# Performance work log

Hardware: AMD Instinct MI355X
Metric: run time of the kernel (lower is better)

## Reference

```python
import jax, jax.numpy as jnp
import numpy as np
import math

D_MODEL = 1024
NHEAD = 16
SEQ_LEN = 4096
K_PROJ = 16
HEAD_DIM = D_MODEL // NHEAD


def setup_inputs() -> dict:
    key = jax.random.key(0)
    ks = jax.random.split(key, 11)
    x = jax.random.normal(ks[0], (4, SEQ_LEN, D_MODEL), dtype=jnp.float32)
    s = 1.0 / math.sqrt(D_MODEL)
    Wq = jax.random.uniform(ks[1], (D_MODEL, D_MODEL), minval=-s, maxval=s)
    bq = jax.random.uniform(ks[2], (D_MODEL,), minval=-s, maxval=s)
    Wk = jax.random.uniform(ks[3], (D_MODEL, D_MODEL), minval=-s, maxval=s)
    bk = jax.random.uniform(ks[4], (D_MODEL,), minval=-s, maxval=s)
    Wv = jax.random.uniform(ks[5], (D_MODEL, D_MODEL), minval=-s, maxval=s)
    bv = jax.random.uniform(ks[6], (D_MODEL,), minval=-s, maxval=s)
    Wo = jax.random.uniform(ks[7], (D_MODEL, D_MODEL), minval=-s, maxval=s)
    bo = jax.random.uniform(ks[8], (D_MODEL,), minval=-s, maxval=s)
    E = jax.random.normal(ks[9], (NHEAD, K_PROJ, SEQ_LEN)) * 0.02
    F = jax.random.normal(ks[10], (NHEAD, K_PROJ, SEQ_LEN)) * 0.02
    return {"x": x, "Wq": Wq, "bq": bq, "Wk": Wk, "bk": bk,
            "Wv": Wv, "bv": bv, "Wo": Wo, "bo": bo, "E": E, "F": F}


def reference(x, Wq, bq, Wk, bk, Wv, bv, Wo, bo, E, F):
    B, N, D = x.shape
    # torch Linear: y = x @ W.T + b
    q = x @ Wq.T + bq
    k = x @ Wk.T + bk
    v = x @ Wv.T + bv
    # [B, H, N, Dh]
    def split_heads(t):
        return t.reshape(B, N, NHEAD, HEAD_DIM).transpose(0, 2, 1, 3)
    q, k, v = split_heads(q), split_heads(k), split_heads(v)
    # low-rank projections of K, V along sequence: [B, H, Kp, Dh]
    k_lin = jnp.einsum('bhnd,hkn->bhkd', k, E)
    v_lin = jnp.einsum('bhnd,hkn->bhkd', v, F)
    scores = jnp.einsum('bhnd,bhkd->bhnk', q, k_lin) / math.sqrt(HEAD_DIM)
    attn = jax.nn.softmax(scores, axis=-1)  # dropout is identity in eval
    out = jnp.einsum('bhnk,bhkd->bhnd', attn, v_lin)
    out = out.transpose(0, 2, 1, 3).reshape(B, N, D)
    return out @ Wo.T + bo
```

## Files before the change

### kernel.cpp

```cpp
#include <hip/hip_runtime.h>
#include <hip/hip_bf16.h>

#define SEQLEN 4096

typedef __bf16 bf16x8 __attribute__((ext_vector_type(8)));
typedef float f32x4 __attribute__((ext_vector_type(4)));
typedef __attribute__((ext_vector_type(8))) unsigned short u16x8;

__device__ inline float bf2f(unsigned short s) {
  union { unsigned u; float f; } t; t.u = ((unsigned)s) << 16; return t.f;
}
__device__ inline unsigned short f2bf(float f) {
  __hip_bfloat16 h = __float2bfloat16(f);
  return *reinterpret_cast<unsigned short*>(&h);
}

__device__ inline void gload_lds16(const void* g, void* l) {
  __builtin_amdgcn_global_load_lds(
      (const __attribute__((address_space(1))) unsigned int*)g,
      (__attribute__((address_space(3))) unsigned int*)l, 16, 0, 0);
}

__global__ void cvt_all(const float* __restrict__ x, const float* __restrict__ Wq,
                        const float* __restrict__ Wk, const float* __restrict__ Wv,
                        const float* __restrict__ Wo,
                        const float* __restrict__ bq, const float* __restrict__ bk,
                        const float* __restrict__ bv,
                        unsigned short* __restrict__ Xb,
                        unsigned short* __restrict__ Wqkv,
                        unsigned short* __restrict__ WoB, float* __restrict__ Bqkv) {
  long i = (long)blockIdx.x * 256 + threadIdx.x;
  const float* src;
  unsigned short* dst;
  long rel;
  if (i < 4194304) {
    src = x; dst = Xb; rel = i;
  } else if (i < 4456448) {
    src = Wq; dst = Wqkv; rel = i - 4194304;
  } else if (i < 4718592) {
    src = Wk; dst = Wqkv + 1048576; rel = i - 4456448;
  } else if (i < 4980736) {
    src = Wv; dst = Wqkv + 2097152; rel = i - 4718592;
  } else if (i < 5242880) {
    src = Wo; dst = WoB; rel = i - 4980736;
  } else if (i < 5243648) {
    long j = i - 5242880;
    const float* bsrc = (j < 256) ? bq : (j < 512) ? bk : bv;
    long jr = j & 255;
    reinterpret_cast<float4*>(Bqkv)[j] =
        reinterpret_cast<const float4*>(bsrc)[jr];
    return;
  } else {
    return;
  }
  float4 v = reinterpret_cast<const float4*>(src)[rel];
  ushort4 o;
  o.x = f2bf(v.x); o.y = f2bf(v.y); o.z = f2bf(v.z); o.w = f2bf(v.w);
  reinterpret_cast<ushort4*>(dst)[rel] = o;
}


#define MFMA16(mk, A00, A01, A10, A11)                                          \
  __builtin_amdgcn_s_setprio(1);                                                \
  _Pragma("unroll")                                                             \
  for (int n = 0; n < 4; ++n)                                                   \
    acc[2*(mk)][n]   = __builtin_amdgcn_mfma_f32_16x16x32_bf16(A00, b[n][0], acc[2*(mk)][n],   0, 0, 0); \
  _Pragma("unroll")                                                             \
  for (int n = 0; n < 4; ++n)                                                   \
    acc[2*(mk)+1][n] = __builtin_amdgcn_mfma_f32_16x16x32_bf16(A10, b[n][0], acc[2*(mk)+1][n], 0, 0, 0); \
  _Pragma("unroll")                                                             \
  for (int n = 0; n < 4; ++n)                                                   \
    acc[2*(mk)][n]   = __builtin_amdgcn_mfma_f32_16x16x32_bf16(A01, b[n][1], acc[2*(mk)][n],   0, 0, 0); \
  _Pragma("unroll")                                                             \
  for (int n = 0; n < 4; ++n)                                                   \
    acc[2*(mk)+1][n] = __builtin_amdgcn_mfma_f32_16x16x32_bf16(A11, b[n][1], acc[2*(mk)+1][n], 0, 0, 0); \
  __builtin_amdgcn_s_setprio(0);

#define LDA8(mi, sg) (*reinterpret_cast<const bf16x8*>(&as[((wr << 7) + (mi) * 16 + r16) * 64 + (sg) * 8]))
#define LDB8(ni, sg) (*reinterpret_cast<const bf16x8*>(&bs[((wc << 6) + (ni) * 16 + r16) * 64 + (sg) * 8]))

template <typename OUT_T>
__global__ __launch_bounds__(512, 2) void gemm8p(
    const unsigned short* __restrict__ A, const unsigned short* __restrict__ B,
    const float* __restrict__ bias, OUT_T* __restrict__ C, int M, int N, int K,
    int ldc) {
  extern __shared__ __align__(16) unsigned short lds[];

  const int tid = threadIdx.x;
  const int lane = tid & 63, wv = tid >> 6;
  const int wr = wv >> 2, wc = wv & 3;
  const int r16 = lane & 15, kg = lane >> 4;
  const int sg0 = (0 * 4 + kg) ^ (r16 & 7);
  const int sg1 = (1 * 4 + kg) ^ (r16 & 7);

  const int xcd = (int)blockIdx.x & 7;
  const int pos = (int)blockIdx.x >> 3;
  const int rpx = (M >> 8) >> 3;
  const int tile_m = xcd * rpx + (pos % rpx);
  const int tile_n = pos / rpx;
  const int brow = tile_m << 8, bcol = tile_n << 8;

  const unsigned short* Ag = A + (size_t)brow * K;
  const unsigned short* Bg = B + (size_t)bcol * K;

  const int sr = tid >> 3;
  const int sc = tid & 7;
  const int sgl = sc ^ (sr & 7);

  auto STG = [&](const unsigned short* G, unsigned short* dstbuf, int row0, int kt) {
    gload_lds16(G + (size_t)(row0 + sr) * K + (size_t)kt * 64 + sgl * 8,
                dstbuf + (row0 + sr) * 64 + sc * 8);
  };

  f32x4 acc[8][4];
#pragma unroll
  for (int m = 0; m < 8; ++m)
#pragma unroll
    for (int n = 0; n < 4; ++n) acc[m][n] = (f32x4)0.0f;

  {
    unsigned short* a0 = lds;
    unsigned short* b0 = lds + 32768;
    STG(Bg, b0, 0, 0);   STG(Bg, b0, 64, 0);
    STG(Bg, b0, 128, 0); STG(Bg, b0, 192, 0);
    STG(Ag, a0, 0, 0);   STG(Ag, a0, 128, 0);
    STG(Ag, a0, 64, 0);  STG(Ag, a0, 192, 0);
  }
  asm volatile("s_waitcnt vmcnt(2)" ::: "memory");
  __builtin_amdgcn_s_barrier();

  const int NT = K >> 6;
  for (int t = 0; t < NT; ++t) {
    const int cur = t & 1;
    const unsigned short* as = lds + (cur << 14);
    const unsigned short* bs = lds + 32768 + (cur << 14);
    unsigned short* an = lds + ((cur ^ 1) << 14);
    unsigned short* bn = lds + 32768 + ((cur ^ 1) << 14);
    const int tn = (t + 1 < NT) ? t + 1 : 0;

    bf16x8 b[4][2];
#pragma unroll
    for (int n = 0; n < 4; ++n) { b[n][0] = LDB8(n, sg0); b[n][1] = LDB8(n, sg1); }

    {
      bf16x8 a00 = LDA8(0, sg0), a01 = LDA8(0, sg1);
      bf16x8 a10 = LDA8(1, sg0), a11 = LDA8(1, sg1);
      STG(Bg, bn, 0, tn);   STG(Bg, bn, 64, tn);
      STG(Bg, bn, 128, tn); STG(Bg, bn, 192, tn);
      __builtin_amdgcn_s_barrier();
      MFMA16(0, a00, a01, a10, a11);
      __builtin_amdgcn_s_barrier();
    }
    {
      bf16x8 a00 = LDA8(2, sg0), a01 = LDA8(2, sg1);
      bf16x8 a10 = LDA8(3, sg0), a11 = LDA8(3, sg1);
      STG(Ag, an, 0, tn); STG(Ag, an, 128, tn);
      __builtin_amdgcn_s_barrier();
      MFMA16(1, a00, a01, a10, a11);
      asm volatile("s_waitcnt vmcnt(6)" ::: "memory");
      __builtin_amdgcn_s_barrier();
    }
    {
      bf16x8 a00 = LDA8(4, sg0), a01 = LDA8(4, sg1);
      bf16x8 a10 = LDA8(5, sg0), a11 = LDA8(5, sg1);
      STG(Ag, an, 64, tn); STG(Ag, an, 192, tn);
      __builtin_amdgcn_s_barrier();
      MFMA16(2, a00, a01, a10, a11);
      __builtin_amdgcn_s_barrier();
    }
    {
      bf16x8 a00 = LDA8(6, sg0), a01 = LDA8(6, sg1);
      bf16x8 a10 = LDA8(7, sg0), a11 = LDA8(7, sg1);
      __builtin_amdgcn_s_barrier();
      MFMA16(3, a00, a01, a10, a11);
      asm volatile("s_waitcnt vmcnt(2)" ::: "memory");
      __builtin_amdgcn_s_barrier();
    }
  }
  asm volatile("s_waitcnt vmcnt(0)" ::: "memory");

  if constexpr (sizeof(OUT_T) == 2) {
    __builtin_amdgcn_s_barrier();
    unsigned short* C2 = reinterpret_cast<unsigned short*>(C);
    float bvs[4];
#pragma unroll
    for (int n = 0; n < 4; ++n)
      bvs[n] = bias ? bias[bcol + wc * 64 + n * 16 + r16] : 0.0f;
#pragma unroll
    for (int m = 0; m < 8; ++m) {
#pragma unroll
      for (int r = 0; r < 4; ++r) {
        int rw = m * 16 + kg * 4 + r;
        int xo = (rw & 12) << 2;
#pragma unroll
        for (int n = 0; n < 4; ++n) {
          lds[wv * 8192 + rw * 64 + ((n * 16 + r16) ^ xo)] =
              f2bf(acc[m][n][r] + bvs[n]);
        }
      }
    }
    __syncthreads();
#pragma unroll
    for (int p = 0; p < 16; ++p) {
      int grow = p * 16 + (tid >> 5);
      int g = tid & 31;
      int wvs = ((grow >> 7) << 2) + (g >> 3);
      int row_l = grow & 127;
      int src = wvs * 8192 + row_l * 64 + (((g & 7) * 8) ^ ((row_l & 12) << 2));
      u16x8 vv = *reinterpret_cast<const u16x8*>(&lds[src]);
      *reinterpret_cast<u16x8*>(&C2[(size_t)(brow + grow) * ldc + bcol + g * 8]) = vv;
    }
  } else {
#pragma unroll
    for (int n = 0; n < 4; ++n) {
      int col = bcol + wc * 64 + n * 16 + r16;
      float bv = bias ? bias[col] : 0.0f;
#pragma unroll
      for (int m = 0; m < 8; ++m) {
#pragma unroll
        for (int r = 0; r < 4; ++r) {
          int row = brow + wr * 128 + m * 16 + kg * 4 + r;
          C[(size_t)row * ldc + col] = acc[m][n][r] + bv;
        }
      }
    }
  }
}

__global__ void kvlin_part(const unsigned short* __restrict__ qkv,
                           const float* __restrict__ E, const float* __restrict__ F,
                           float* __restrict__ part) {
  __shared__ __align__(16) unsigned short Ks[128 * 64], Vs[128 * 64];
  __shared__ __align__(16) float Es[16 * 128], Fs[16 * 128];
  const int tid = threadIdx.x;
  const int bid = blockIdx.x;
  const int bh = bid >> 3, ns = bid & 7;
  const int b = bh >> 4, h = bh & 15;
  const int d = tid & 63, kk = tid >> 6;
  float aK[4] = {0, 0, 0, 0}, aV[4] = {0, 0, 0, 0};
  for (int c = 0; c < 4; ++c) {
    int n0 = ns * 512 + c * 128;
#pragma unroll
    for (int it = 0; it < 4; ++it) {
      int f = it * 256 + tid;
      int row = f >> 3, ch = f & 7;
      const unsigned short* gk =
          qkv + (size_t)(b * SEQLEN + n0 + row) * 3072 + 1024 + h * 64 + ch * 8;
      gload_lds16(gk, &Ks[f * 8]);
      gload_lds16(gk + 1024, &Vs[f * 8]);
    }
#pragma unroll
    for (int it = 0; it < 2; ++it) {
      int f = it * 256 + tid;
      int k = f >> 5, ch = f & 31;
      const float* ge = E + (size_t)(h * 16 + k) * SEQLEN + n0 + ch * 4;
      const float* gf = F + (size_t)(h * 16 + k) * SEQLEN + n0 + ch * 4;
      gload_lds16(ge, &Es[f * 4]);
      gload_lds16(gf, &Fs[f * 4]);
    }
    __syncthreads();
    for (int n = 0; n < 128; ++n) {
      float kv = bf2f(Ks[n * 64 + d]);
      float vv = bf2f(Vs[n * 64 + d]);
#pragma unroll
      for (int j = 0; j < 4; ++j) {
        aK[j] += Es[(kk * 4 + j) * 128 + n] * kv;
        aV[j] += Fs[(kk * 4 + j) * 128 + n] * vv;
      }
    }
    __syncthreads();
  }
  size_t base = ((size_t)ns * 64 + bh) * 2048;
#pragma unroll
  for (int j = 0; j < 4; ++j) {
    part[base + (kk * 4 + j) * 64 + d] = aK[j];
    part[base + 1024 + (kk * 4 + j) * 64 + d] = aV[j];
  }
}

__global__ void kvlin_reduce(const float* __restrict__ part, float* __restrict__ out) {
  int i = blockIdx.x * 256 + threadIdx.x;
  float s = 0;
#pragma unroll
  for (int ns = 0; ns < 8; ++ns) s += part[(size_t)ns * 131072 + i];
  out[i] = s;
}

__global__ void attn_kernel(const unsigned short* __restrict__ qkv,
                            const float* __restrict__ kvlin,
                            unsigned short* __restrict__ aout) {
  __shared__ float kl[1024], vl[1024];
  const int tid = threadIdx.x;
  const int bid = blockIdx.x;
  const int bh = bid >> 4, nt = bid & 15;
  const int b = bh >> 4, h = bh & 15;
  for (int i = tid; i < 1024; i += 256) {
    kl[i] = kvlin[(size_t)bh * 2048 + i];
    vl[i] = kvlin[(size_t)bh * 2048 + 1024 + i];
  }
  __syncthreads();
  const int n = nt * 256 + tid;
  const unsigned short* qp = qkv + (size_t)(b * SEQLEN + n) * 3072 + h * 64;
  float q[64];
#pragma unroll
  for (int c2 = 0; c2 < 8; ++c2) {
    u16x8 v = *reinterpret_cast<const u16x8*>(qp + c2 * 8);
#pragma unroll
    for (int j = 0; j < 8; ++j) q[c2 * 8 + j] = bf2f(v[j]);
  }
  float s[16];
#pragma unroll
  for (int k = 0; k < 16; ++k) {
    float a = 0;
#pragma unroll
    for (int dd = 0; dd < 64; ++dd) a += q[dd] * kl[k * 64 + dd];
    s[k] = a * 0.125f;
  }
  float mx = s[0];
#pragma unroll
  for (int k = 1; k < 16; ++k) mx = fmaxf(mx, s[k]);
  float sum = 0;
#pragma unroll
  for (int k = 0; k < 16; ++k) { s[k] = __expf(s[k] - mx); sum += s[k]; }
  float inv = 1.0f / sum;
#pragma unroll
  for (int k = 0; k < 16; ++k) s[k] *= inv;
  unsigned short* op = aout + (size_t)(b * SEQLEN + n) * 1024 + h * 64;
#pragma unroll
  for (int d0 = 0; d0 < 8; ++d0) {
    float o[8] = {0, 0, 0, 0, 0, 0, 0, 0};
#pragma unroll
    for (int k = 0; k < 16; ++k) {
      float p = s[k];
#pragma unroll
      for (int j = 0; j < 8; ++j) o[j] += p * vl[k * 64 + d0 * 8 + j];
    }
    u16x8 pk;
#pragma unroll
    for (int j = 0; j < 8; ++j) pk[j] = f2bf(o[j]);
    *reinterpret_cast<u16x8*>(op + d0 * 8) = pk;
  }
}

extern "C" void kernel_launch(void* const* d_in, const int* in_sizes, int n_in,
                              void* d_out, int out_size, void* d_ws, size_t ws_size,
                              hipStream_t stream) {
  const float* x  = (const float*)d_in[0];
  const float* Wq = (const float*)d_in[1];
  const float* bq = (const float*)d_in[2];
  const float* Wk = (const float*)d_in[3];
  const float* bk = (const float*)d_in[4];
  const float* Wv = (const float*)d_in[5];
  const float* bv = (const float*)d_in[6];
  const float* Wo = (const float*)d_in[7];
  const float* bo = (const float*)d_in[8];
  const float* E  = (const float*)d_in[9];
  const float* F  = (const float*)d_in[10];
  float* out = (float*)d_out;

  char* ws = (char*)d_ws;
  unsigned short* Xb   = (unsigned short*)(ws);
  unsigned short* Wqkv = (unsigned short*)(ws + 33554432);
  unsigned short* WoB  = (unsigned short*)(ws + 39845888);
  float*          Bqkv = (float*)(ws + 41943040);
  unsigned short* QKV  = (unsigned short*)(ws + 41955328);
  float*          KVp  = (float*)(ws + 142618624);
  float*          KVl  = (float*)(ws + 146812928);
  unsigned short* AOut = Xb;

  (void)hipFuncSetAttribute(reinterpret_cast<const void*>(gemm8p<unsigned short>),
                            hipFuncAttributeMaxDynamicSharedMemorySize, 131072);
  (void)hipFuncSetAttribute(reinterpret_cast<const void*>(gemm8p<float>),
                            hipFuncAttributeMaxDynamicSharedMemorySize, 131072);

  cvt_all<<<20483, 256, 0, stream>>>(x, Wq, Wk, Wv, Wo, bq, bk, bv,
                                     Xb, Wqkv, WoB, Bqkv);

  gemm8p<unsigned short><<<768, 512, 131072, stream>>>(
      Xb, Wqkv, Bqkv, QKV, 16384, 3072, 1024, 3072);

  kvlin_part<<<512, 256, 0, stream>>>(QKV, E, F, KVp);
  kvlin_reduce<<<512, 256, 0, stream>>>(KVp, KVl);
  attn_kernel<<<1024, 256, 0, stream>>>(QKV, KVl, AOut);

  gemm8p<float><<<256, 512, 131072, stream>>>(
      AOut, WoB, bo, out, 16384, 1024, 1024, 1024);
}
```

Measured before the change: 253.4 us.

## Restructure GEMM main loop into quadrant MFMA phases with deeper prefetch

The 256x256 bf16 GEMM main loop now splits each wave's work into four quadrants (two M halves by two N halves) with register reuse of A and B fragments across phases. Global-to-LDS staging is reorganised so half-tiles for k-step t+2 are issued while computing t, and the column mapping per wave is changed to two 32-wide column groups, with the epilogue and bias indexing updated to match. The goal is more overlap of loads with MFMA work and fewer LDS reads per MFMA, at the cost of more complex vmcnt/lgkmcnt accounting and more live registers.

```diff
diff --git a/kernel.cpp b/kernel.cpp
--- a/kernel.cpp
+++ b/kernel.cpp
@@ -60,24 +60,21 @@
 }
 
 
-#define MFMA16(mk, A00, A01, A10, A11)                                          \
+#define MFMAQ(mh, nh, AR, BR)                                                   \
   __builtin_amdgcn_s_setprio(1);                                                \
   _Pragma("unroll")                                                             \
-  for (int n = 0; n < 4; ++n)                                                   \
-    acc[2*(mk)][n]   = __builtin_amdgcn_mfma_f32_16x16x32_bf16(A00, b[n][0], acc[2*(mk)][n],   0, 0, 0); \
-  _Pragma("unroll")                                                             \
-  for (int n = 0; n < 4; ++n)                                                   \
-    acc[2*(mk)+1][n] = __builtin_amdgcn_mfma_f32_16x16x32_bf16(A10, b[n][0], acc[2*(mk)+1][n], 0, 0, 0); \
-  _Pragma("unroll")                                                             \
-  for (int n = 0; n < 4; ++n)                                                   \
-    acc[2*(mk)][n]   = __builtin_amdgcn_mfma_f32_16x16x32_bf16(A01, b[n][1], acc[2*(mk)][n],   0, 0, 0); \
-  _Pragma("unroll")                                                             \
-  for (int n = 0; n < 4; ++n)                                                   \
-    acc[2*(mk)+1][n] = __builtin_amdgcn_mfma_f32_16x16x32_bf16(A11, b[n][1], acc[2*(mk)+1][n], 0, 0, 0); \
+  for (int ks = 0; ks < 2; ++ks)                                                \
+    _Pragma("unroll")                                                           \
+    for (int mi = 0; mi < 4; ++mi)                                              \
+      _Pragma("unroll")                                                         \
+      for (int ni = 0; ni < 2; ++ni)                                            \
+        acc[(mh) * 4 + mi][(nh) * 2 + ni] =                                     \
+            __builtin_amdgcn_mfma_f32_16x16x32_bf16(                            \
+                AR[mi][ks], BR[ni][ks], acc[(mh) * 4 + mi][(nh) * 2 + ni], 0, 0, 0); \
   __builtin_amdgcn_s_setprio(0);
 
 #define LDA8(mi, sg) (*reinterpret_cast<const bf16x8*>(&as[((wr << 7) + (mi) * 16 + r16) * 64 + (sg) * 8]))
-#define LDB8(ni, sg) (*reinterpret_cast<const bf16x8*>(&bs[((wc << 6) + (ni) * 16 + r16) * 64 + (sg) * 8]))
+#define LDB8N(nh, ni, sg) (*reinterpret_cast<const bf16x8*>(&bs[(((nh) << 7) + (wc << 5) + (ni) * 16 + r16) * 64 + (sg) * 8]))
 
 template <typename OUT_T>
 __global__ __launch_bounds__(512, 2) void gemm8p(
@@ -111,6 +108,14 @@
     gload_lds16(G + (size_t)(row0 + sr) * K + (size_t)kt * 64 + sgl * 8,
                 dstbuf + (row0 + sr) * 64 + sc * 8);
   };
+  auto STGH = [&](int hw, int pb, int kt) {
+    unsigned short* ab = lds + (pb << 14);
+    unsigned short* bb = lds + 32768 + (pb << 14);
+    if (hw == 0)      { STG(Ag, ab, 0, kt);   STG(Ag, ab, 128, kt); }
+    else if (hw == 1) { STG(Bg, bb, 0, kt);   STG(Bg, bb, 64, kt); }
+    else if (hw == 2) { STG(Bg, bb, 128, kt); STG(Bg, bb, 192, kt); }
+    else              { STG(Ag, ab, 64, kt);  STG(Ag, ab, 192, kt); }
+  };
 
   f32x4 acc[8][4];
 #pragma unroll
@@ -118,62 +123,56 @@
 #pragma unroll
     for (int n = 0; n < 4; ++n) acc[m][n] = (f32x4)0.0f;
 
-  {
-    unsigned short* a0 = lds;
-    unsigned short* b0 = lds + 32768;
-    STG(Bg, b0, 0, 0);   STG(Bg, b0, 64, 0);
-    STG(Bg, b0, 128, 0); STG(Bg, b0, 192, 0);
-    STG(Ag, a0, 0, 0);   STG(Ag, a0, 128, 0);
-    STG(Ag, a0, 64, 0);  STG(Ag, a0, 192, 0);
-  }
-  asm volatile("s_waitcnt vmcnt(2)" ::: "memory");
+  const int NT = K >> 6;
+  STGH(0, 0, 0); STGH(1, 0, 0); STGH(2, 0, 0); STGH(3, 0, 0);
+  STGH(0, 1, 1); STGH(1, 1, 1); STGH(2, 1, 1);
+  asm volatile("s_waitcnt vmcnt(6)" ::: "memory");
   __builtin_amdgcn_s_barrier();
 
-  const int NT = K >> 6;
   for (int t = 0; t < NT; ++t) {
     const int cur = t & 1;
     const unsigned short* as = lds + (cur << 14);
     const unsigned short* bs = lds + 32768 + (cur << 14);
-    unsigned short* an = lds + ((cur ^ 1) << 14);
-    unsigned short* bn = lds + 32768 + ((cur ^ 1) << 14);
-    const int tn = (t + 1 < NT) ? t + 1 : 0;
-
-    bf16x8 b[4][2];
-#pragma unroll
-    for (int n = 0; n < 4; ++n) { b[n][0] = LDB8(n, sg0); b[n][1] = LDB8(n, sg1); }
+    const int w1 = (t + 1 < NT) ? t + 1 : 0;
+    const int w2 = (t + 2 < NT) ? t + 2 : t + 2 - NT;
+    const int b1n = (t + 1) & 1;
+
+    bf16x8 a[4][2], b0[2][2], b1[2][2];
 
     {
-      bf16x8 a00 = LDA8(0, sg0), a01 = LDA8(0, sg1);
-      bf16x8 a10 = LDA8(1, sg0), a11 = LDA8(1, sg1);
-      STG(Bg, bn, 0, tn);   STG(Bg, bn, 64, tn);
-      STG(Bg, bn, 128, tn); STG(Bg, bn, 192, tn);
-      __builtin_amdgcn_s_barrier();
-      MFMA16(0, a00, a01, a10, a11);
+#pragma unroll
+      for (int mi = 0; mi < 4; ++mi) { a[mi][0] = LDA8(mi, sg0); a[mi][1] = LDA8(mi, sg1); }
+#pragma unroll
+      for (int ni = 0; ni < 2; ++ni) { b0[ni][0] = LDB8N(0, ni, sg0); b0[ni][1] = LDB8N(0, ni, sg1); }
+      STGH(3, b1n, w1);
+      asm volatile("s_waitcnt lgkmcnt(8)" ::: "memory");
+      __builtin_amdgcn_s_barrier();
+      asm volatile("s_waitcnt lgkmcnt(0)" ::: "memory");
+      MFMAQ(0, 0, a, b0);
       __builtin_amdgcn_s_barrier();
     }
     {
-      bf16x8 a00 = LDA8(2, sg0), a01 = LDA8(2, sg1);
-      bf16x8 a10 = LDA8(3, sg0), a11 = LDA8(3, sg1);
-      STG(Ag, an, 0, tn); STG(Ag, an, 128, tn);
-      __builtin_amdgcn_s_barrier();
-      MFMA16(1, a00, a01, a10, a11);
+#pragma unroll
+      for (int ni = 0; ni < 2; ++ni) { b1[ni][0] = LDB8N(1, ni, sg0); b1[ni][1] = LDB8N(1, ni, sg1); }
+      STGH(0, cur, w2);
+      __builtin_amdgcn_s_barrier();
+      asm volatile("s_waitcnt lgkmcnt(0)" ::: "memory");
+      MFMAQ(0, 1, a, b1);
+      __builtin_amdgcn_s_barrier();
+    }
+    {
+#pragma unroll
+      for (int mi = 0; mi < 4; ++mi) { a[mi][0] = LDA8(4 + mi, sg0); a[mi][1] = LDA8(4 + mi, sg1); }
+      STGH(1, cur, w2);
+      __builtin_amdgcn_s_barrier();
+      asm volatile("s_waitcnt lgkmcnt(0)" ::: "memory");
+      MFMAQ(1, 1, a, b1);
+      __builtin_amdgcn_s_barrier();
+    }
+    {
+      STGH(2, cur, w2);
+      MFMAQ(1, 0, a, b0);
       asm volatile("s_waitcnt vmcnt(6)" ::: "memory");
-      __builtin_amdgcn_s_barrier();
-    }
-    {
-      bf16x8 a00 = LDA8(4, sg0), a01 = LDA8(4, sg1);
-      bf16x8 a10 = LDA8(5, sg0), a11 = LDA8(5, sg1);
-      STG(Ag, an, 64, tn); STG(Ag, an, 192, tn);
-      __builtin_amdgcn_s_barrier();
-      MFMA16(2, a00, a01, a10, a11);
-      __builtin_amdgcn_s_barrier();
-    }
-    {
-      bf16x8 a00 = LDA8(6, sg0), a01 = LDA8(6, sg1);
-      bf16x8 a10 = LDA8(7, sg0), a11 = LDA8(7, sg1);
-      __builtin_amdgcn_s_barrier();
-      MFMA16(3, a00, a01, a10, a11);
-      asm volatile("s_waitcnt vmcnt(2)" ::: "memory");
       __builtin_amdgcn_s_barrier();
     }
   }
@@ -185,7 +184,8 @@
     float bvs[4];
 #pragma unroll
     for (int n = 0; n < 4; ++n)
-      bvs[n] = bias ? bias[bcol + wc * 64 + n * 16 + r16] : 0.0f;
+      bvs[n] = bias ? bias[bcol + ((n >> 1) << 7) + (wc << 5) + ((n & 1) << 4) + r16]
+                    : 0.0f;
 #pragma unroll
     for (int m = 0; m < 8; ++m) {
 #pragma unroll
@@ -204,16 +204,17 @@
     for (int p = 0; p < 16; ++p) {
       int grow = p * 16 + (tid >> 5);
       int g = tid & 31;
-      int wvs = ((grow >> 7) << 2) + (g >> 3);
+      int wvs = ((grow >> 7) << 2) + ((g >> 2) & 3);
       int row_l = grow & 127;
-      int src = wvs * 8192 + row_l * 64 + (((g & 7) * 8) ^ ((row_l & 12) << 2));
+      int c4g = ((g >> 4) << 5) + ((g & 3) << 3);
+      int src = wvs * 8192 + row_l * 64 + (c4g ^ ((row_l & 12) << 2));
       u16x8 vv = *reinterpret_cast<const u16x8*>(&lds[src]);
       *reinterpret_cast<u16x8*>(&C2[(size_t)(brow + grow) * ldc + bcol + g * 8]) = vv;
     }
   } else {
 #pragma unroll
     for (int n = 0; n < 4; ++n) {
-      int col = bcol + wc * 64 + n * 16 + r16;
+      int col = bcol + ((n >> 1) << 7) + (wc << 5) + ((n & 1) << 4) + r16;
       float bv = bias ? bias[col] : 0.0f;
 #pragma unroll
       for (int m = 0; m < 8; ++m) {
```

After: 261.3 us. 1.03x slower.
